# Performance work log

Measured on AMD Instinct MI355X. Metric: run time of the kernel, lower is better.

## Reference

```python
import jax, jax.numpy as jnp
import numpy as np

K_DIM = 64  # contraction dim for scores; scale = 1/sqrt(K_DIM)


def setup_inputs() -> dict:
    key = jax.random.key(0)
    ks = jax.random.split(key, 8)
    B, T, L, D, H, E, V = 128, 16, 32, 256, 8, 64, 64
    return {
        "queries": jax.random.normal(ks[0], (B, T, L, D), dtype=jnp.float32),
        "keys": jax.random.normal(ks[1], (B, T, L, D), dtype=jnp.float32),
        "values": jax.random.normal(ks[2], (B, T, L, D), dtype=jnp.float32),
        "attn_mask": jax.random.uniform(ks[3], (B, B), dtype=jnp.float32),
        "Wq": jax.random.normal(ks[4], (D, H, E), dtype=jnp.float32) * 0.05,
        "Wk": jax.random.normal(ks[5], (D, H, E), dtype=jnp.float32) * 0.05,
        "Wv": jax.random.normal(ks[6], (D, H, V), dtype=jnp.float32) * 0.05,
        "w_head": jax.random.normal(ks[7], (H,), dtype=jnp.float32),
    }


def reference(queries, keys, values, attn_mask, Wq, Wk, Wv, w_head):
    # QKV projections (EinsumDense 'abcd,def->abcef', no bias): [b,t,l,h,e]
    Q = jnp.einsum('btld,dhe->btlhe', queries, Wq)
    K = jnp.einsum('btld,dhe->btlhe', keys, Wk)
    V = jnp.einsum('btld,dhe->btlhe', values, Wv)

    scale = 1.0 / jnp.sqrt(jnp.float32(K_DIM))
    # cross-batch attention scores: [t, l, h, B, b]
    scores = jnp.einsum('Btlhe,btlhe->tlhBb', Q, K) * scale
    # multiplicative mask, broadcast over trailing [B, b]
    scores = scores * attn_mask
    # Dropout is identity at inference (Keras Dropout, training=False)

    attn = jnp.einsum('tlhBb,btlhe->Bthle', jax.nn.softmax(scores, axis=-1), V)
    # head-mixing output ('bthle,h->btle'): [b, t, l, v_dim]
    attn_output = jnp.einsum('bthle,h->btle', attn, w_head)
    return (attn_output, scores)
```

## Files before the change

kernel.cpp:

```cpp
#include <hip/hip_runtime.h>
#include <hip/hip_bf16.h>


using bf16x8 = __attribute__((ext_vector_type(8))) __bf16;
using f32x4  = __attribute__((ext_vector_type(4))) float;

__device__ __forceinline__ f32x4 mfma16(bf16x8 a, bf16x8 b, f32x4 c) {
  return __builtin_amdgcn_mfma_f32_16x16x32_bf16(a, b, c, 0, 0, 0);
}

__global__ __launch_bounds__(512) void k0_wt(const float* __restrict__ Wq,
                                             const float* __restrict__ Wk,
                                             const float* __restrict__ Wv,
                                             __bf16* __restrict__ Wt) {
  int f   = blockIdx.x * 512 + threadIdx.x;
  int mat = f >> 14;
  int rem = f & 16383;
  int d8  = rem >> 9;
  int col = rem & 511;
  const float* W = (mat == 0) ? Wq : (mat == 1) ? Wk : Wv;
  bf16x8 v;
#pragma unroll
  for (int i = 0; i < 8; ++i) v[i] = (__bf16)W[(d8 * 8 + i) * 512 + col];
  *(bf16x8*)(Wt + mat * 131072 + col * 256 + d8 * 8) = v;
}

__global__ __launch_bounds__(512) void k1_proj(const float* __restrict__ xq,
                                               const float* __restrict__ xk,
                                               const float* __restrict__ xv,
                                               const __bf16* __restrict__ Wt,
                                               __bf16* __restrict__ qkv) {
  __shared__ char smem[98304];
  const int tid  = threadIdx.x;
  const int tl   = blockIdx.x;
  const int lane = tid & 63, w = tid >> 6;
  const int lrow = lane & 15, lk = lane >> 4;
  const int rs = w >> 1, cs = w & 1;
  const f32x4 z4 = {0.f, 0.f, 0.f, 0.f};

  for (int m = 0; m < 3; ++m) {
    const float* xm = (m == 0) ? xq : (m == 1) ? xk : xv;
    __syncthreads();
#pragma unroll
    for (int i = 0; i < 8; ++i) {
      int c = i * 512 + tid;
      int row = c >> 5, sl = c & 31;
      const float* g = xm + (size_t)row * 131072 + (size_t)tl * 256 + sl * 8;
      float4 f0 = *(const float4*)g;
      float4 f1 = *(const float4*)(g + 4);
      bf16x8 v;
      v[0] = (__bf16)f0.x; v[1] = (__bf16)f0.y; v[2] = (__bf16)f0.z; v[3] = (__bf16)f0.w;
      v[4] = (__bf16)f1.x; v[5] = (__bf16)f1.y; v[6] = (__bf16)f1.z; v[7] = (__bf16)f1.w;
      *(bf16x8*)(smem + row * 512 + ((sl ^ (row & 7)) << 4)) = v;
    }
    for (int h = 0; h < 8; ++h) {
      __syncthreads();
#pragma unroll
      for (int i = 0; i < 4; ++i) {
        int c = i * 512 + tid;
        int wrow = c >> 5, sl = c & 31;
        uint4 val = *(const uint4*)(Wt + (size_t)(m * 512 + h * 64 + wrow) * 256 + sl * 8);
        *(uint4*)(smem + 65536 + wrow * 512 + ((sl ^ (wrow & 7)) << 4)) = val;
      }
      __syncthreads();

      f32x4 acc[2][2];
#pragma unroll
      for (int ri = 0; ri < 2; ++ri)
#pragma unroll
        for (int ci = 0; ci < 2; ++ci) acc[ri][ci] = z4;

#pragma unroll
      for (int kk = 0; kk < 8; ++kk) {
        int koff = lk * 16 + kk * 64;
        bf16x8 a[2], b[2];
#pragma unroll
        for (int ri = 0; ri < 2; ++ri) {
          int row = rs * 32 + ri * 16 + lrow;
          a[ri] = *(const bf16x8*)(smem + row * 512 + (koff ^ ((row & 7) << 4)));
        }
#pragma unroll
        for (int ci = 0; ci < 2; ++ci) {
          int col = cs * 32 + ci * 16 + lrow;
          b[ci] = *(const bf16x8*)(smem + 65536 + col * 512 + (koff ^ ((col & 7) << 4)));
        }
#pragma unroll
        for (int ri = 0; ri < 2; ++ri)
#pragma unroll
          for (int ci = 0; ci < 2; ++ci)
            acc[ri][ci] = mfma16(a[ri], b[ci], acc[ri][ci]);
      }

      __bf16* dst = qkv + (size_t)(tl * 8 + h) * 32768 + m * 8192;
#pragma unroll
      for (int ri = 0; ri < 2; ++ri)
#pragma unroll
        for (int ci = 0; ci < 2; ++ci)
#pragma unroll
          for (int r = 0; r < 4; ++r) {
            int brow = rs * 32 + ri * 16 + lk * 4 + r;
            int e    = cs * 32 + ci * 16 + lrow;
            dst[brow * 64 + e] = (__bf16)acc[ri][ci][r];
          }
    }
  }
}

__global__ __launch_bounds__(512) void k2_attn(const float* __restrict__ mask,
                                               const float* __restrict__ w_head,
                                               float* out_base) {
  __shared__ char smem[81920];
  const int tid  = threadIdx.x;
  const int tl   = blockIdx.x;
  const int lane = tid & 63, w = tid >> 6;
  const int lrow = lane & 15, lk = lane >> 4;
  const f32x4 z4 = {0.f, 0.f, 0.f, 0.f};

  float* scores = out_base + 4194304;

  float mreg[8][4];
#pragma unroll
  for (int ct = 0; ct < 8; ++ct)
#pragma unroll
    for (int r = 0; r < 4; ++r)
      mreg[ct][r] = mask[(w * 16 + lk * 4 + r) * 128 + ct * 16 + lrow];

  f32x4 oacc[4];
#pragma unroll
  for (int i = 0; i < 4; ++i) oacc[i] = z4;

  for (int h = 0; h < 8; ++h) {
    const __bf16* slot = (const __bf16*)scores + (size_t)(tl * 8 + h) * 32768;
    float wh = w_head[h];
    __syncthreads();
#pragma unroll
    for (int i = 0; i < 2; ++i) {
      int c = i * 512 + tid;
      int row = c >> 3, sl = c & 7;
      uint4 qv = *(const uint4*)(slot + row * 64 + sl * 8);
      *(uint4*)(smem + row * 128 + ((sl ^ (row & 7)) << 4)) = qv;
      uint4 kv = *(const uint4*)(slot + 8192 + row * 64 + sl * 8);
      *(uint4*)(smem + 16384 + row * 128 + ((sl ^ (row & 7)) << 4)) = kv;
      bf16x8 vv = *(const bf16x8*)(slot + 16384 + row * 64 + sl * 8);
#pragma unroll
      for (int j = 0; j < 8; ++j) {
        int e = sl * 8 + j;
        *(__bf16*)(smem + 32768 + e * 256 + ((row * 2) ^ ((e & 7) << 4))) = vv[j];
      }
    }
    __syncthreads();

    int arow = w * 16 + lrow;
    const char* qb = smem + arow * 128;
    int aswz = (arow & 7) << 4;
    bf16x8 a0 = *(const bf16x8*)(qb + ((lk * 16 + 0) ^ aswz));
    bf16x8 a1 = *(const bf16x8*)(qb + ((lk * 16 + 64) ^ aswz));
    f32x4 sacc[8];
#pragma unroll
    for (int ct = 0; ct < 8; ++ct) {
      int bcol = ct * 16 + lrow;
      const char* kb = smem + 16384 + bcol * 128;
      int bswz = (bcol & 7) << 4;
      bf16x8 b0 = *(const bf16x8*)(kb + ((lk * 16 + 0) ^ bswz));
      bf16x8 b1 = *(const bf16x8*)(kb + ((lk * 16 + 64) ^ bswz));
      sacc[ct] = mfma16(a0, b0, z4);
      sacc[ct] = mfma16(a1, b1, sacc[ct]);
    }

    float* srow = scores + (size_t)(tl * 8 + h) * 16384;
#pragma unroll
    for (int ct = 0; ct < 8; ++ct)
#pragma unroll
      for (int r = 0; r < 4; ++r) {
        float s = sacc[ct][r] * 0.125f * mreg[ct][r];
        sacc[ct][r] = s;
        srow[(w * 16 + lk * 4 + r) * 128 + ct * 16 + lrow] = s;
      }

#pragma unroll
    for (int r = 0; r < 4; ++r) {
      float mx = sacc[0][r];
#pragma unroll
      for (int ct = 1; ct < 8; ++ct) mx = fmaxf(mx, sacc[ct][r]);
      mx = fmaxf(mx, __shfl_xor(mx, 1));
      mx = fmaxf(mx, __shfl_xor(mx, 2));
      mx = fmaxf(mx, __shfl_xor(mx, 4));
      mx = fmaxf(mx, __shfl_xor(mx, 8));
      float sum = 0.f;
#pragma unroll
      for (int ct = 0; ct < 8; ++ct) {
        float p = __expf(sacc[ct][r] - mx);
        sacc[ct][r] = p;
        sum += p;
      }
      sum += __shfl_xor(sum, 1);
      sum += __shfl_xor(sum, 2);
      sum += __shfl_xor(sum, 4);
      sum += __shfl_xor(sum, 8);
      float fct = wh / sum;
      int row16 = lk * 4 + r;
      char* pb = smem + 49152 + w * 4096 + row16 * 256;
      int pswz = (row16 & 7) << 4;
#pragma unroll
      for (int ct = 0; ct < 8; ++ct) {
        int col = ct * 16 + lrow;
        *(__bf16*)(pb + ((col * 2) ^ pswz)) = (__bf16)(sacc[ct][r] * fct);
      }
    }

    const char* pab = smem + 49152 + w * 4096 + lrow * 256;
    int paswz = (lrow & 7) << 4;
    bf16x8 pa[4];
#pragma unroll
    for (int kk = 0; kk < 4; ++kk)
      pa[kk] = *(const bf16x8*)(pab + ((lk * 16 + kk * 64) ^ paswz));
#pragma unroll
    for (int ct2 = 0; ct2 < 4; ++ct2) {
      int ecol = ct2 * 16 + lrow;
      const char* vb = smem + 32768 + ecol * 256;
      int vswz = (ecol & 7) << 4;
#pragma unroll
      for (int kk = 0; kk < 4; ++kk) {
        bf16x8 b = *(const bf16x8*)(vb + ((lk * 16 + kk * 64) ^ vswz));
        oacc[ct2] = mfma16(pa[kk], b, oacc[ct2]);
      }
    }
  }

#pragma unroll
  for (int ct2 = 0; ct2 < 4; ++ct2)
#pragma unroll
    for (int r = 0; r < 4; ++r) {
      int brow = w * 16 + lk * 4 + r;
      int e    = ct2 * 16 + lrow;
      out_base[(size_t)(brow * 512 + tl) * 64 + e] = oacc[ct2][r];
    }
}

extern "C" void kernel_launch(void* const* d_in, const int* in_sizes, int n_in,
                              void* d_out, int out_size, void* d_ws, size_t ws_size,
                              hipStream_t stream) {
  const float* q    = (const float*)d_in[0];
  const float* k    = (const float*)d_in[1];
  const float* v    = (const float*)d_in[2];
  const float* mask = (const float*)d_in[3];
  const float* Wq   = (const float*)d_in[4];
  const float* Wk   = (const float*)d_in[5];
  const float* Wv   = (const float*)d_in[6];
  const float* wh   = (const float*)d_in[7];
  float* out = (float*)d_out;

  __bf16* Wt  = (__bf16*)out;
  __bf16* qkv = (__bf16*)(out + 4194304);

  hipLaunchKernelGGL(k0_wt,   dim3(96),  dim3(512), 0, stream, Wq, Wk, Wv, Wt);
  hipLaunchKernelGGL(k1_proj, dim3(512), dim3(512), 0, stream, q, k, v, Wt, qkv);
  hipLaunchKernelGGL(k2_attn, dim3(512), dim3(512), 0, stream, mask, wh, out);
}
```

Measured before the change: 264.7 us.

## Split projection kernel across Q/K/V grid dimension and give each wave one head

The projection kernel now launches a 512x3 grid, with one block per (t,l) slice and per matrix, instead of looping over the three matrices inside each block. Within a block, each of the eight waves owns one head and computes a 128x64 output tile in two row halves. The weight tiles are read directly from global memory into registers rather than staged through shared memory, which removes the per-head barriers and the shared-memory weight buffer. In exchange, weight reads rely on L2/L1 caching, and each thread holds a larger 4x4 accumulator tile, which raises register pressure.

Result: faster. 235.2 us (-11.1%).

```diff
diff --git a/kernel.cpp b/kernel.cpp
--- a/kernel.cpp
+++ b/kernel.cpp
@@ -30,79 +30,70 @@
                                                const float* __restrict__ xv,
                                                const __bf16* __restrict__ Wt,
                                                __bf16* __restrict__ qkv) {
-  __shared__ char smem[98304];
+  __shared__ char smem[65536];
   const int tid  = threadIdx.x;
   const int tl   = blockIdx.x;
+  const int m    = blockIdx.y;
   const int lane = tid & 63, w = tid >> 6;
   const int lrow = lane & 15, lk = lane >> 4;
-  const int rs = w >> 1, cs = w & 1;
   const f32x4 z4 = {0.f, 0.f, 0.f, 0.f};
 
-  for (int m = 0; m < 3; ++m) {
-    const float* xm = (m == 0) ? xq : (m == 1) ? xk : xv;
-    __syncthreads();
-#pragma unroll
-    for (int i = 0; i < 8; ++i) {
-      int c = i * 512 + tid;
-      int row = c >> 5, sl = c & 31;
-      const float* g = xm + (size_t)row * 131072 + (size_t)tl * 256 + sl * 8;
-      float4 f0 = *(const float4*)g;
-      float4 f1 = *(const float4*)(g + 4);
-      bf16x8 v;
-      v[0] = (__bf16)f0.x; v[1] = (__bf16)f0.y; v[2] = (__bf16)f0.z; v[3] = (__bf16)f0.w;
-      v[4] = (__bf16)f1.x; v[5] = (__bf16)f1.y; v[6] = (__bf16)f1.z; v[7] = (__bf16)f1.w;
-      *(bf16x8*)(smem + row * 512 + ((sl ^ (row & 7)) << 4)) = v;
-    }
-    for (int h = 0; h < 8; ++h) {
-      __syncthreads();
-#pragma unroll
-      for (int i = 0; i < 4; ++i) {
-        int c = i * 512 + tid;
-        int wrow = c >> 5, sl = c & 31;
-        uint4 val = *(const uint4*)(Wt + (size_t)(m * 512 + h * 64 + wrow) * 256 + sl * 8);
-        *(uint4*)(smem + 65536 + wrow * 512 + ((sl ^ (wrow & 7)) << 4)) = val;
-      }
-      __syncthreads();
-
-      f32x4 acc[2][2];
-#pragma unroll
-      for (int ri = 0; ri < 2; ++ri)
-#pragma unroll
-        for (int ci = 0; ci < 2; ++ci) acc[ri][ci] = z4;
-
-#pragma unroll
-      for (int kk = 0; kk < 8; ++kk) {
-        int koff = lk * 16 + kk * 64;
-        bf16x8 a[2], b[2];
-#pragma unroll
-        for (int ri = 0; ri < 2; ++ri) {
-          int row = rs * 32 + ri * 16 + lrow;
-          a[ri] = *(const bf16x8*)(smem + row * 512 + (koff ^ ((row & 7) << 4)));
+  const float* xm = (m == 0) ? xq : (m == 1) ? xk : xv;
+
+#pragma unroll
+  for (int i = 0; i < 8; ++i) {
+    int c = i * 512 + tid;
+    int row = c >> 5, sl = c & 31;
+    const float* g = xm + (size_t)row * 131072 + (size_t)tl * 256 + sl * 8;
+    float4 f0 = *(const float4*)g;
+    float4 f1 = *(const float4*)(g + 4);
+    bf16x8 v;
+    v[0] = (__bf16)f0.x; v[1] = (__bf16)f0.y; v[2] = (__bf16)f0.z; v[3] = (__bf16)f0.w;
+    v[4] = (__bf16)f1.x; v[5] = (__bf16)f1.y; v[6] = (__bf16)f1.z; v[7] = (__bf16)f1.w;
+    *(bf16x8*)(smem + row * 512 + ((sl ^ (row & 7)) << 4)) = v;
+  }
+  __syncthreads();
+
+  const int h = w;
+  const __bf16* wbase = Wt + (size_t)(m * 512 + h * 64) * 256;
+  __bf16* dst = qkv + (size_t)(tl * 8 + h) * 32768 + m * 8192;
+
+  for (int rh = 0; rh < 2; ++rh) {
+    f32x4 acc[4][4];
+#pragma unroll
+    for (int ri = 0; ri < 4; ++ri)
+#pragma unroll
+      for (int ci = 0; ci < 4; ++ci) acc[ri][ci] = z4;
+
+#pragma unroll
+    for (int kk = 0; kk < 8; ++kk) {
+      int koff = lk * 16 + kk * 64;
+      bf16x8 a[4], b[4];
+#pragma unroll
+      for (int ri = 0; ri < 4; ++ri) {
+        int row = rh * 64 + ri * 16 + lrow;
+        a[ri] = *(const bf16x8*)(smem + row * 512 + (koff ^ ((row & 7) << 4)));
+      }
+#pragma unroll
+      for (int ci = 0; ci < 4; ++ci)
+        b[ci] = *(const bf16x8*)(wbase + (ci * 16 + lrow) * 256 + kk * 32 + lk * 8);
+#pragma unroll
+      for (int ri = 0; ri < 4; ++ri)
+#pragma unroll
+        for (int ci = 0; ci < 4; ++ci)
+          acc[ri][ci] = mfma16(a[ri], b[ci], acc[ri][ci]);
+    }
+
+#pragma unroll
+    for (int ri = 0; ri < 4; ++ri)
+#pragma unroll
+      for (int ci = 0; ci < 4; ++ci)
+#pragma unroll
+        for (int r = 0; r < 4; ++r) {
+          int brow = rh * 64 + ri * 16 + lk * 4 + r;
+          int e    = ci * 16 + lrow;
+          dst[brow * 64 + e] = (__bf16)acc[ri][ci][r];
         }
-#pragma unroll
-        for (int ci = 0; ci < 2; ++ci) {
-          int col = cs * 32 + ci * 16 + lrow;
-          b[ci] = *(const bf16x8*)(smem + 65536 + col * 512 + (koff ^ ((col & 7) << 4)));
-        }
-#pragma unroll
-        for (int ri = 0; ri < 2; ++ri)
-#pragma unroll
-          for (int ci = 0; ci < 2; ++ci)
-            acc[ri][ci] = mfma16(a[ri], b[ci], acc[ri][ci]);
-      }
-
-      __bf16* dst = qkv + (size_t)(tl * 8 + h) * 32768 + m * 8192;
-#pragma unroll
-      for (int ri = 0; ri < 2; ++ri)
-#pragma unroll
-        for (int ci = 0; ci < 2; ++ci)
-#pragma unroll
-          for (int r = 0; r < 4; ++r) {
-            int brow = rs * 32 + ri * 16 + lk * 4 + r;
-            int e    = cs * 32 + ci * 16 + lrow;
-            dst[brow * 64 + e] = (__bf16)acc[ri][ci][r];
-          }
-    }
   }
 }
 
@@ -253,7 +244,7 @@
   __bf16* Wt  = (__bf16*)out;
   __bf16* qkv = (__bf16*)(out + 4194304);
 
-  hipLaunchKernelGGL(k0_wt,   dim3(96),  dim3(512), 0, stream, Wq, Wk, Wv, Wt);
-  hipLaunchKernelGGL(k1_proj, dim3(512), dim3(512), 0, stream, q, k, v, Wt, qkv);
-  hipLaunchKernelGGL(k2_attn, dim3(512), dim3(512), 0, stream, mask, wh, out);
-}
+  hipLaunchKernelGGL(k0_wt,   dim3(96),       dim3(512), 0, stream, Wq, Wk, Wv, Wt);
+  hipLaunchKernelGGL(k1_proj, dim3(512, 3),   dim3(512), 0, stream, q, k, v, Wt, qkv);
+  hipLaunchKernelGGL(k2_attn, dim3(512),      dim3(512), 0, stream, mask, wh, out);
+}
```
